# Performance work log

Hardware: AMD Instinct MI355X
Metric: run time of the kernel (lower is better)

The kernel has to match this reference:

```python
import jax, jax.numpy as jnp
import numpy as np

B, EMB, H, G, F, CH, O, OC, KT = 4096, 256, 256, 8, 96, 16, 5, 10, 5
BN_EPS = 1e-3


def _grouped_linear(x, w):
    # x: [B, I], w: [G, I//G, O//G] -> [B, O]
    b = x.shape[0]
    g, ig, og = w.shape
    xg = x.reshape(b, g, ig)
    return jnp.einsum('bgi,gio->bgo', xg, w).reshape(b, g * og)


def _gru_cell(x, h, k, rk, bias):
    # keras GRUCell, reset_after=True; gate order z, r, h; bias: [2, 3H]
    xs = x @ k + bias[0]
    hs = h @ rk + bias[1]
    xz, xr, xh = jnp.split(xs, 3, axis=-1)
    hz, hr, hh = jnp.split(hs, 3, axis=-1)
    z = jax.nn.sigmoid(xz + hz)
    r = jax.nn.sigmoid(xr + hr)
    cand = jnp.tanh(xh + r * hh)
    return z * h + (1.0 - z) * cand


def setup_inputs() -> dict:
    key = jax.random.key(0)
    ks = jax.random.split(key, 20)
    w = lambda i, shape: (jax.random.normal(ks[i], shape, dtype=jnp.float32) * 0.05)
    inp = {
        'emb': jax.random.normal(ks[0], (B, EMB), dtype=jnp.float32),
        'c0': jax.random.normal(ks[1], (B, 1, F, CH), dtype=jnp.float32),
        'df_dec_state': jax.random.normal(ks[2], (B, 2 * H), dtype=jnp.float32),
        'df_convp_buf': jax.random.normal(ks[3], (B, KT - 1, F, CH), dtype=jnp.float32),
        'w_in': w(4, (G, EMB // G, H // G)),
        'gru_k0': w(5, (H, 3 * H)),
        'gru_rk0': w(6, (H, 3 * H)),
        'gru_b0': w(7, (2, 3 * H)),
        'gru_k1': w(8, (H, 3 * H)),
        'gru_rk1': w(9, (H, 3 * H)),
        'gru_b1': w(10, (2, 3 * H)),
        'w_out': w(11, (G, H // G, (F * OC) // G)),
        'fc_a_w': w(12, (H, 1)),
        'fc_a_b': jnp.zeros((1,), dtype=jnp.float32),
        'conv_w': w(13, (KT, 1, CH // 2, OC)),  # grouped conv, groups=gcd(16,10)=2
        'pw_w': w(14, (OC, OC)),                # 1x1 pointwise, no bias
        'bn_gamma': jnp.ones((OC,), dtype=jnp.float32),
        'bn_beta': jnp.zeros((OC,), dtype=jnp.float32),
        'bn_mean': jnp.zeros((OC,), dtype=jnp.float32),
        'bn_var': jnp.ones((OC,), dtype=jnp.float32),
    }
    return inp


def reference(emb, c0, df_dec_state, df_convp_buf,
              w_in, gru_k0, gru_rk0, gru_b0, gru_k1, gru_rk1, gru_b1,
              w_out, fc_a_w, fc_a_b, conv_w, pw_w,
              bn_gamma, bn_beta, bn_mean, bn_var):
    b = emb.shape[0]
    # SqueezedGRUStep: grouped linear in-proj + ReLU
    x_in = jax.nn.relu(_grouped_linear(emb, w_in))  # [B, H]
    h0 = df_dec_state[:, :H]
    h1 = df_dec_state[:, H:]
    out0 = _gru_cell(x_in, h0, gru_k0, gru_rk0, gru_b0)
    out1 = _gru_cell(out0, h1, gru_k1, gru_rk1, gru_b1)
    new_state = jnp.concatenate([out0, out1], axis=-1)  # [B, 2H]
    c = out1 + x_in  # gru_skip = identity

    # causal conv step: concat buffer + current frame -> [B, KT, F, CH]
    x = jnp.concatenate([df_convp_buf, c0], axis=1)
    new_buf = x[:, 1:, :, :]
    # grouped conv (groups=2), kernel (KT,1), valid over the KT frames -> last frame
    xg = x.reshape(b, KT, F, 2, CH // 2)                 # [B,T,F,g,i]
    wg = conv_w.reshape(KT, CH // 2, 2, OC // 2)         # [T,i,g,o]
    y = jnp.einsum('btfgi,tigo->bfgo', xg, wg).reshape(b, F, OC)
    # separable pointwise 1x1 conv
    y = y @ pw_w
    # batch norm (inference) + relu
    inv = jax.lax.rsqrt(bn_var + BN_EPS)
    y = (y - bn_mean) * inv * bn_gamma + bn_beta
    c0_out = jax.nn.relu(y)                              # [B, F, OC]

    alpha = jax.nn.sigmoid(emb @ jnp.zeros_like(fc_a_w) + c @ fc_a_w + fc_a_b)  # [B,1]
    c_out = jnp.tanh(_grouped_linear(c, w_out)).reshape(b, F, OC)
    c_out = c_out + c0_out
    # DfOutputReshapeMF: [B,1,F,O*2] -> [B,O,1,F,2]
    coefs = c_out.reshape(b, 1, F, O, 2).transpose(0, 3, 1, 2, 4)
    return (coefs, alpha, new_state, new_buf)
```

## Files before the change

### kernel.cpp

```cpp
#include <hip/hip_runtime.h>

typedef unsigned short u16;
typedef __attribute__((ext_vector_type(8))) u16 u16x8;
typedef __attribute__((ext_vector_type(8))) __bf16 bf16x8;
typedef __attribute__((ext_vector_type(4))) float f32x4;

#define ALPHA_OFF   3932160
#define NST_OFF     3936256
#define NBUF_OFF    6033408

__device__ __forceinline__ u16 f2bf(float f) {
  unsigned u = __builtin_bit_cast(unsigned, f);
  u += 0x7fffu + ((u >> 16) & 1u);
  return (u16)(u >> 16);
}
__device__ __forceinline__ float fsig(float x) { return 1.f / (1.f + __expf(-x)); }
__device__ __forceinline__ float ftanh(float x) {
  x = fminf(15.f, fmaxf(-15.f, x));
  float e = __expf(2.f * x);
  return (e - 1.f) / (e + 1.f);
}
__device__ __forceinline__ f32x4 mfma16(u16x8 a, u16x8 b, f32x4 c) {
  return __builtin_amdgcn_mfma_f32_16x16x32_bf16(
      __builtin_bit_cast(bf16x8, a), __builtin_bit_cast(bf16x8, b), c, 0, 0, 0);
}

__global__ __launch_bounds__(256) void wprep_kernel(
    const float* __restrict__ k0, const float* __restrict__ rk0,
    const float* __restrict__ k1, const float* __restrict__ rk1,
    u16* __restrict__ kT) {
  __shared__ u16 tl[64][65];
  int nb = blockIdx.x, kb = blockIdx.y, m = blockIdx.z;
  const float* src = (m == 0) ? k0 : (m == 1) ? rk0 : (m == 2) ? k1 : rk1;
  u16* dst = kT + (size_t)m * 768 * 256;
  int tid = threadIdx.x;
  int c = tid & 63, r4 = tid >> 6;
  for (int rr = 0; rr < 64; rr += 4) {
    int k = kb * 64 + rr + r4, n = nb * 64 + c;
    tl[rr + r4][c] = f2bf(src[(size_t)k * 768 + n]);
  }
  __syncthreads();
  for (int rr = 0; rr < 64; rr += 4) {
    int n = nb * 64 + rr + r4, k = kb * 64 + c;
    dst[(size_t)n * 256 + k] = tl[c][rr + r4];
  }
}

__global__ __launch_bounds__(256) void prep_kernel(
    const float* __restrict__ emb, const float* __restrict__ dec,
    const float* __restrict__ w_in,
    float* __restrict__ x_f32, u16* __restrict__ x_q,
    u16* __restrict__ h0q, u16* __restrict__ h1q) {
  __shared__ float wl[8192];
  __shared__ float el[16][256];
  int tid = threadIdx.x, rowBase = blockIdx.x * 16;
  for (int i = tid; i < 8192; i += 256) wl[i] = w_in[i];
  for (int i = tid; i < 4096; i += 256)
    el[i >> 8][i & 255] = emb[(size_t)(rowBase + (i >> 8)) * 256 + (i & 255)];
  __syncthreads();
  int g = tid >> 5, o = tid & 31;
  for (int r = 0; r < 16; ++r) {
    float acc = 0.f;
#pragma unroll
    for (int i = 0; i < 32; ++i) acc += el[r][g * 32 + i] * wl[g * 1024 + i * 32 + o];
    acc = fmaxf(acc, 0.f);
    size_t p = (size_t)(rowBase + r) * 256 + tid;
    x_f32[p] = acc;
    x_q[p] = f2bf(acc);
  }
  for (int i = tid; i < 8192; i += 256) {
    int r = i >> 9, c = i & 511;
    float v = dec[(size_t)(rowBase + r) * 512 + c];
    if (c < 256) h0q[(size_t)(rowBase + r) * 256 + c] = f2bf(v);
    else         h1q[(size_t)(rowBase + r) * 256 + (c - 256)] = f2bf(v);
  }
}

template <int LAYER>
__global__ __launch_bounds__(256) void gru_kernel(
    const u16* __restrict__ xq, const u16* __restrict__ hq,
    const float* __restrict__ dec,
    const u16* __restrict__ kT, const u16* __restrict__ rkT,
    const float* __restrict__ bias,
    float* __restrict__ nst,
    u16* __restrict__ outq,
    const float* __restrict__ x_f32,
    float* __restrict__ c_f32) {
  __shared__ u16 lsA[2][32][40];
  __shared__ u16 lsB[2][192][40];
  int tid = threadIdx.x;
  int wave = tid >> 6, lane = tid & 63;
  int m0 = lane & 15, quad = lane >> 4;
  int rowBase = blockIdx.x * 32;
  int jz = blockIdx.y * 64;
  int cw = wave * 16;
  f32x4 az0 = {0.f, 0.f, 0.f, 0.f}, az1 = az0, ar0 = az0, ar1 = az0;
  f32x4 axh0 = az0, axh1 = az0, ahh0 = az0, ahh1 = az0;

  for (int kk = 0; kk < 8; ++kk) {
    int k0 = kk * 32;
    __syncthreads();
#pragma unroll
    for (int it = 0; it < 7; ++it) {
      int idx = tid + it * 256;
      const u16* src;
      u16* dst;
      if (idx < 256) {
        int mat = idx >> 7, r = (idx >> 2) & 31, c4 = idx & 3;
        src = (mat ? hq : xq) + (size_t)(rowBase + r) * 256 + k0 + c4 * 8;
        dst = &lsA[mat][r][c4 * 8];
      } else {
        int j = idx - 256;
        int mat = (j >= 768);
        int jm = mat ? j - 768 : j;
        int rB = jm >> 2, c4 = jm & 3;
        int n = (rB >> 6) * 256 + jz + (rB & 63);
        src = (mat ? rkT : kT) + (size_t)n * 256 + k0 + c4 * 8;
        dst = &lsB[mat][rB][c4 * 8];
      }
      *(uint4*)dst = *(const uint4*)src;
    }
    __syncthreads();
    u16x8 ax0v = *(const u16x8*)&lsA[0][m0][quad * 8];
    u16x8 ax1v = *(const u16x8*)&lsA[0][16 + m0][quad * 8];
    u16x8 ah0v = *(const u16x8*)&lsA[1][m0][quad * 8];
    u16x8 ah1v = *(const u16x8*)&lsA[1][16 + m0][quad * 8];
    u16x8 bkz = *(const u16x8*)&lsB[0][cw + m0][quad * 8];
    u16x8 bkr = *(const u16x8*)&lsB[0][64 + cw + m0][quad * 8];
    u16x8 bkh = *(const u16x8*)&lsB[0][128 + cw + m0][quad * 8];
    u16x8 brz = *(const u16x8*)&lsB[1][cw + m0][quad * 8];
    u16x8 brr = *(const u16x8*)&lsB[1][64 + cw + m0][quad * 8];
    u16x8 brh = *(const u16x8*)&lsB[1][128 + cw + m0][quad * 8];
    az0 = mfma16(ax0v, bkz, az0);  az0 = mfma16(ah0v, brz, az0);
    az1 = mfma16(ax1v, bkz, az1);  az1 = mfma16(ah1v, brz, az1);
    ar0 = mfma16(ax0v, bkr, ar0);  ar0 = mfma16(ah0v, brr, ar0);
    ar1 = mfma16(ax1v, bkr, ar1);  ar1 = mfma16(ah1v, brr, ar1);
    axh0 = mfma16(ax0v, bkh, axh0); axh1 = mfma16(ax1v, bkh, axh1);
    ahh0 = mfma16(ah0v, brh, ahh0); ahh1 = mfma16(ah1v, brh, ahh1);
  }

  int col = jz + cw + m0;
  float bz = bias[col] + bias[768 + col];
  float br = bias[256 + col] + bias[1024 + col];
  float bxh = bias[512 + col];
  float bhh = bias[1280 + col];
  const int hoff = LAYER ? 256 : 0;
#pragma unroll
  for (int t = 0; t < 2; ++t) {
    f32x4 vz = t ? az1 : az0, vr = t ? ar1 : ar0;
    f32x4 vxh = t ? axh1 : axh0, vhh = t ? ahh1 : ahh0;
#pragma unroll
    for (int i = 0; i < 4; ++i) {
      int row = rowBase + t * 16 + quad * 4 + i;
      float h = dec[(size_t)row * 512 + hoff + col];
      float z = fsig(vz[i] + bz);
      float r = fsig(vr[i] + br);
      float cand = ftanh(vxh[i] + bxh + r * (vhh[i] + bhh));
      float o = z * h + (1.f - z) * cand;
      nst[(size_t)row * 512 + hoff + col] = o;
      if (LAYER == 0) {
        outq[(size_t)row * 256 + col] = f2bf(o);
      } else {
        float c = o + x_f32[(size_t)row * 256 + col];
        c_f32[(size_t)row * 256 + col] = c;
      }
    }
  }
}

__global__ __launch_bounds__(256) void wout_kernel(
    const float* __restrict__ c_f32, const float* __restrict__ w_out,
    float* __restrict__ outc) {
  __shared__ float cs[16][256];
  int tid = threadIdx.x, rowBase = blockIdx.x * 16;
  for (int i = tid; i < 4096; i += 256)
    cs[i >> 8][i & 255] = c_f32[(size_t)(rowBase + (i >> 8)) * 256 + (i & 255)];
  __syncthreads();
  for (int flat = tid; flat < 960; flat += 256) {
    int g = flat / 120, og = flat % 120;
    float acc[16];
#pragma unroll
    for (int r = 0; r < 16; ++r) acc[r] = 0.f;
    for (int i = 0; i < 32; ++i) {
      float w = w_out[(size_t)g * 3840 + i * 120 + og];
#pragma unroll
      for (int r = 0; r < 16; ++r) acc[r] += cs[r][g * 32 + i] * w;
    }
#pragma unroll
    for (int r = 0; r < 16; ++r)
      outc[(size_t)(rowBase + r) * 960 + flat] = ftanh(acc[r]);
  }
}

__global__ __launch_bounds__(256) void head_kernel(
    const float* __restrict__ convp, const float* __restrict__ c0,
    const float* __restrict__ c_f32,
    const float* __restrict__ conv_w, const float* __restrict__ pw_w,
    const float* __restrict__ bng, const float* __restrict__ bnb,
    const float* __restrict__ bnm, const float* __restrict__ bnv,
    const float* __restrict__ fca_w, const float* __restrict__ fca_b,
    float* __restrict__ outp) {
  __shared__ float xs[5 * 96 * 16];
  __shared__ float cs[256];
  __shared__ float ybuf[96][10];
  __shared__ float cw[400];
  __shared__ float pw[100];
  __shared__ float bscale[10], bshift[10];
  __shared__ float fca[256];
  __shared__ float ared[4];
  int tid = threadIdx.x, lane = tid & 63, wave = tid >> 6;
  for (int i = tid; i < 400; i += 256) cw[i] = conv_w[i];
  if (tid < 100) pw[tid] = pw_w[tid];
  if (tid < 10) {
    float s = bng[tid] * rsqrtf(bnv[tid] + 1e-3f);
    bscale[tid] = s;
    bshift[tid] = bnb[tid] - bnm[tid] * s;
  }
  fca[tid] = fca_w[tid];
  float4* nb4 = (float4*)(outp + NBUF_OFF);
  const float4* cp4 = (const float4*)convp;
  const float4* c04 = (const float4*)c0;

  for (int rr = 0; rr < 2; ++rr) {
    int b = blockIdx.x * 2 + rr;
    __syncthreads();
    for (int i = tid; i < 1920; i += 256) {
      int t = i / 384, p = i % 384;
      float4 v = (t < 4) ? cp4[(size_t)b * 1536 + i] : c04[(size_t)b * 384 + p];
      ((float4*)xs)[i] = v;
      if (t >= 1) nb4[(size_t)b * 1536 + (size_t)(t - 1) * 384 + p] = v;
    }
    if (tid < 64) ((float4*)cs)[tid] = ((const float4*)c_f32)[(size_t)b * 64 + tid];
    __syncthreads();
    for (int u = tid; u < 960; u += 256) {
      int f = u / 10, oc = u % 10;
      int xo = (oc >= 5) ? 8 : 0;
      float acc = 0.f;
#pragma unroll
      for (int t = 0; t < 5; ++t)
#pragma unroll
        for (int i = 0; i < 8; ++i)
          acc += xs[t * 1536 + f * 16 + xo + i] * cw[t * 80 + i * 10 + oc];
      ybuf[f][oc] = acc;
    }
    float ap = cs[tid] * fca[tid];
#pragma unroll
    for (int off = 32; off > 0; off >>= 1) ap += __shfl_down(ap, off, 64);
    if (lane == 0) ared[wave] = ap;
    __syncthreads();
    if (tid == 0)
      outp[ALPHA_OFF + b] = fsig(ared[0] + ared[1] + ared[2] + ared[3] + fca_b[0]);
    float vals[4];
    int nv = 0;
    for (int u2 = tid; u2 < 480; u2 += 256) {
      int o = u2 / 96, f = u2 % 96;
#pragma unroll
      for (int q = 0; q < 2; ++q) {
        int p = o * 2 + q;
        float y2 = 0.f;
#pragma unroll
        for (int j = 0; j < 10; ++j) y2 += ybuf[f][j] * pw[j * 10 + p];
        float bnr = fmaxf(y2 * bscale[p] + bshift[p], 0.f);
        float wt = outp[(size_t)b * 960 + f * 10 + p];
        vals[nv++] = bnr + wt;
      }
    }
    __syncthreads();
    nv = 0;
    for (int u2 = tid; u2 < 480; u2 += 256) {
      int o = u2 / 96, f = u2 % 96;
      outp[(size_t)b * 960 + o * 192 + f * 2 + 0] = vals[nv++];
      outp[(size_t)b * 960 + o * 192 + f * 2 + 1] = vals[nv++];
    }
  }
}

extern "C" void kernel_launch(void* const* d_in, const int* in_sizes, int n_in,
                              void* d_out, int out_size, void* d_ws, size_t ws_size,
                              hipStream_t stream) {
  const float* emb    = (const float*)d_in[0];
  const float* c0     = (const float*)d_in[1];
  const float* dec    = (const float*)d_in[2];
  const float* convp  = (const float*)d_in[3];
  const float* w_in   = (const float*)d_in[4];
  const float* gk0    = (const float*)d_in[5];
  const float* grk0   = (const float*)d_in[6];
  const float* gb0    = (const float*)d_in[7];
  const float* gk1    = (const float*)d_in[8];
  const float* grk1   = (const float*)d_in[9];
  const float* gb1    = (const float*)d_in[10];
  const float* w_out  = (const float*)d_in[11];
  const float* fca_w  = (const float*)d_in[12];
  const float* fca_b  = (const float*)d_in[13];
  const float* conv_w = (const float*)d_in[14];
  const float* pw_w   = (const float*)d_in[15];
  const float* bng    = (const float*)d_in[16];
  const float* bnb    = (const float*)d_in[17];
  const float* bnm    = (const float*)d_in[18];
  const float* bnv    = (const float*)d_in[19];
  float* out = (float*)d_out;
  char* ws = (char*)d_ws;
  float* x_f32 = (float*)(ws + 0);
  float* c_f32 = (float*)(ws + 4194304);
  u16*   x_q   = (u16*)(ws + 8388608);
  u16*   h0q   = (u16*)(ws + 10485760);
  u16*   h1q   = (u16*)(ws + 12582912);
  u16*   o0q   = (u16*)(ws + 14680064);
  u16*   kT    = (u16*)(ws + 16777216);

  wprep_kernel<<<dim3(12, 4, 4), 256, 0, stream>>>(gk0, grk0, gk1, grk1, kT);
  prep_kernel<<<dim3(256), 256, 0, stream>>>(emb, dec, w_in, x_f32, x_q, h0q, h1q);
  gru_kernel<0><<<dim3(128, 4), 256, 0, stream>>>(x_q, h0q, dec, kT, kT + 196608,
                                                  gb0, out + NST_OFF, o0q, nullptr, nullptr);
  gru_kernel<1><<<dim3(128, 4), 256, 0, stream>>>(o0q, h1q, dec, kT + 2 * 196608, kT + 3 * 196608,
                                                  gb1, out + NST_OFF, nullptr, x_f32, c_f32);
  wout_kernel<<<dim3(256), 256, 0, stream>>>(c_f32, w_out, out);
  head_kernel<<<dim3(2048), 256, 0, stream>>>(convp, c0, c_f32, conv_w, pw_w,
                                              bng, bnb, bnm, bnv, fca_w, fca_b, out);
}
```

Before: 346.4 us.

## Concatenate GRU K-dim, double-buffer via global_load_lds, bf16 conv staging

The input and recurrent weights are concatenated along K into one [768,512] bf16 matrix per layer. Activations are packed as [x|h] rows, so the GRU GEMM becomes a single K=512 loop with 64-row tiles, double-buffered through direct global-to-LDS loads. The fp32 x copy is dropped and the skip connection reads the bf16 x instead, which adds rounding error. The head kernel moves to one batch row per block, stages the conv input as bf16 in LDS and restructures the conv so each thread computes five outputs.

Result: slower. 357.3 us (+3.1%).

```diff
diff --git a/kernel.cpp b/kernel.cpp
--- a/kernel.cpp
+++ b/kernel.cpp
@@ -13,6 +13,9 @@
   unsigned u = __builtin_bit_cast(unsigned, f);
   u += 0x7fffu + ((u >> 16) & 1u);
   return (u16)(u >> 16);
+}
+__device__ __forceinline__ float bf2f(u16 v) {
+  return __builtin_bit_cast(float, (unsigned)v << 16);
 }
 __device__ __forceinline__ float fsig(float x) { return 1.f / (1.f + __expf(-x)); }
 __device__ __forceinline__ float ftanh(float x) {
@@ -24,33 +27,36 @@
   return __builtin_amdgcn_mfma_f32_16x16x32_bf16(
       __builtin_bit_cast(bf16x8, a), __builtin_bit_cast(bf16x8, b), c, 0, 0, 0);
 }
+__device__ __forceinline__ void gload16(const void* g, void* l) {
+  __builtin_amdgcn_global_load_lds(
+      (const __attribute__((address_space(1))) void*)g,
+      (__attribute__((address_space(3))) void*)l, 16, 0, 0);
+}
 
 __global__ __launch_bounds__(256) void wprep_kernel(
-    const float* __restrict__ k0, const float* __restrict__ rk0,
-    const float* __restrict__ k1, const float* __restrict__ rk1,
-    u16* __restrict__ kT) {
+    const float* __restrict__ gk0, const float* __restrict__ grk0,
+    const float* __restrict__ gk1, const float* __restrict__ grk1,
+    u16* __restrict__ W2) {
   __shared__ u16 tl[64][65];
-  int nb = blockIdx.x, kb = blockIdx.y, m = blockIdx.z;
-  const float* src = (m == 0) ? k0 : (m == 1) ? rk0 : (m == 2) ? k1 : rk1;
-  u16* dst = kT + (size_t)m * 768 * 256;
-  int tid = threadIdx.x;
-  int c = tid & 63, r4 = tid >> 6;
+  int nb = blockIdx.x, kb = blockIdx.y, L = blockIdx.z;
+  const float* src = (kb < 4) ? (L ? gk1 : gk0) : (L ? grk1 : grk0);
+  int kbase = (kb & 3) * 64;
+  u16* dst = W2 + (size_t)L * 768 * 512;
+  int tid = threadIdx.x, c = tid & 63, r4 = tid >> 6;
   for (int rr = 0; rr < 64; rr += 4) {
-    int k = kb * 64 + rr + r4, n = nb * 64 + c;
+    int k = kbase + rr + r4, n = nb * 64 + c;
     tl[rr + r4][c] = f2bf(src[(size_t)k * 768 + n]);
   }
   __syncthreads();
   for (int rr = 0; rr < 64; rr += 4) {
     int n = nb * 64 + rr + r4, k = kb * 64 + c;
-    dst[(size_t)n * 256 + k] = tl[c][rr + r4];
+    dst[(size_t)n * 512 + k] = tl[c][rr + r4];
   }
 }
 
 __global__ __launch_bounds__(256) void prep_kernel(
     const float* __restrict__ emb, const float* __restrict__ dec,
-    const float* __restrict__ w_in,
-    float* __restrict__ x_f32, u16* __restrict__ x_q,
-    u16* __restrict__ h0q, u16* __restrict__ h1q) {
+    const float* __restrict__ w_in, u16* __restrict__ A0, u16* __restrict__ A1) {
   __shared__ float wl[8192];
   __shared__ float el[16][256];
   int tid = threadIdx.x, rowBase = blockIdx.x * 16;
@@ -63,80 +69,70 @@
     float acc = 0.f;
 #pragma unroll
     for (int i = 0; i < 32; ++i) acc += el[r][g * 32 + i] * wl[g * 1024 + i * 32 + o];
-    acc = fmaxf(acc, 0.f);
-    size_t p = (size_t)(rowBase + r) * 256 + tid;
-    x_f32[p] = acc;
-    x_q[p] = f2bf(acc);
+    A0[(size_t)(rowBase + r) * 512 + tid] = f2bf(fmaxf(acc, 0.f));
   }
   for (int i = tid; i < 8192; i += 256) {
     int r = i >> 9, c = i & 511;
-    float v = dec[(size_t)(rowBase + r) * 512 + c];
-    if (c < 256) h0q[(size_t)(rowBase + r) * 256 + c] = f2bf(v);
-    else         h1q[(size_t)(rowBase + r) * 256 + (c - 256)] = f2bf(v);
+    u16 q = f2bf(dec[(size_t)(rowBase + r) * 512 + c]);
+    if (c < 256) A0[(size_t)(rowBase + r) * 512 + 256 + c] = q;
+    else         A1[(size_t)(rowBase + r) * 512 + c] = q;
   }
 }
 
 template <int LAYER>
 __global__ __launch_bounds__(256) void gru_kernel(
-    const u16* __restrict__ xq, const u16* __restrict__ hq,
+    const u16* __restrict__ Ain,
+    const u16* __restrict__ W2,
     const float* __restrict__ dec,
-    const u16* __restrict__ kT, const u16* __restrict__ rkT,
     const float* __restrict__ bias,
     float* __restrict__ nst,
-    u16* __restrict__ outq,
-    const float* __restrict__ x_f32,
+    u16* __restrict__ a1out,
+    const u16* __restrict__ xbf,
     float* __restrict__ c_f32) {
-  __shared__ u16 lsA[2][32][40];
-  __shared__ u16 lsB[2][192][40];
-  int tid = threadIdx.x;
-  int wave = tid >> 6, lane = tid & 63;
+  __shared__ __align__(16) u16 lsA[2][64][32];
+  __shared__ __align__(16) u16 lsB[2][3][64][32];
+  int tid = threadIdx.x, lane = tid & 63, wave = tid >> 6;
   int m0 = lane & 15, quad = lane >> 4;
-  int rowBase = blockIdx.x * 32;
-  int jz = blockIdx.y * 64;
-  int cw = wave * 16;
-  f32x4 az0 = {0.f, 0.f, 0.f, 0.f}, az1 = az0, ar0 = az0, ar1 = az0;
-  f32x4 axh0 = az0, axh1 = az0, ahh0 = az0, ahh1 = az0;
-
-  for (int kk = 0; kk < 8; ++kk) {
-    int k0 = kk * 32;
+  int rowBase = blockIdx.x * 64, jz = blockIdx.y * 64, cw = wave * 16;
+  f32x4 acc[4][4];
+#pragma unroll
+  for (int gi = 0; gi < 4; ++gi)
+#pragma unroll
+    for (int rb = 0; rb < 4; ++rb) acc[gi][rb] = (f32x4){0.f, 0.f, 0.f, 0.f};
+
+  int rS = tid >> 2, qS = tid & 3;
+  auto stage = [&](int buf, int k0) {
+    gload16(Ain + (size_t)(rowBase + rS) * 512 + k0 + qS * 8, &lsA[buf][rS][qS * 8]);
+#pragma unroll
+    for (int g = 0; g < 3; ++g)
+      gload16(W2 + (size_t)(g * 256 + jz + rS) * 512 + k0 + qS * 8,
+              &lsB[buf][g][rS][qS * 8]);
+  };
+
+  stage(0, 0);
+  for (int step = 0; step < 16; ++step) {
     __syncthreads();
-#pragma unroll
-    for (int it = 0; it < 7; ++it) {
-      int idx = tid + it * 256;
-      const u16* src;
-      u16* dst;
-      if (idx < 256) {
-        int mat = idx >> 7, r = (idx >> 2) & 31, c4 = idx & 3;
-        src = (mat ? hq : xq) + (size_t)(rowBase + r) * 256 + k0 + c4 * 8;
-        dst = &lsA[mat][r][c4 * 8];
-      } else {
-        int j = idx - 256;
-        int mat = (j >= 768);
-        int jm = mat ? j - 768 : j;
-        int rB = jm >> 2, c4 = jm & 3;
-        int n = (rB >> 6) * 256 + jz + (rB & 63);
-        src = (mat ? rkT : kT) + (size_t)n * 256 + k0 + c4 * 8;
-        dst = &lsB[mat][rB][c4 * 8];
-      }
-      *(uint4*)dst = *(const uint4*)src;
-    }
-    __syncthreads();
-    u16x8 ax0v = *(const u16x8*)&lsA[0][m0][quad * 8];
-    u16x8 ax1v = *(const u16x8*)&lsA[0][16 + m0][quad * 8];
-    u16x8 ah0v = *(const u16x8*)&lsA[1][m0][quad * 8];
-    u16x8 ah1v = *(const u16x8*)&lsA[1][16 + m0][quad * 8];
-    u16x8 bkz = *(const u16x8*)&lsB[0][cw + m0][quad * 8];
-    u16x8 bkr = *(const u16x8*)&lsB[0][64 + cw + m0][quad * 8];
-    u16x8 bkh = *(const u16x8*)&lsB[0][128 + cw + m0][quad * 8];
-    u16x8 brz = *(const u16x8*)&lsB[1][cw + m0][quad * 8];
-    u16x8 brr = *(const u16x8*)&lsB[1][64 + cw + m0][quad * 8];
-    u16x8 brh = *(const u16x8*)&lsB[1][128 + cw + m0][quad * 8];
-    az0 = mfma16(ax0v, bkz, az0);  az0 = mfma16(ah0v, brz, az0);
-    az1 = mfma16(ax1v, bkz, az1);  az1 = mfma16(ah1v, brz, az1);
-    ar0 = mfma16(ax0v, bkr, ar0);  ar0 = mfma16(ah0v, brr, ar0);
-    ar1 = mfma16(ax1v, bkr, ar1);  ar1 = mfma16(ah1v, brr, ar1);
-    axh0 = mfma16(ax0v, bkh, axh0); axh1 = mfma16(ax1v, bkh, axh1);
-    ahh0 = mfma16(ah0v, brh, ahh0); ahh1 = mfma16(ah1v, brh, ahh1);
+    if (step < 15) stage((step & 1) ^ 1, (step + 1) * 32);
+    int cur = step & 1;
+    u16x8 av[4], bv[3];
+#pragma unroll
+    for (int rb = 0; rb < 4; ++rb)
+      av[rb] = *(const u16x8*)&lsA[cur][rb * 16 + m0][quad * 8];
+#pragma unroll
+    for (int g = 0; g < 3; ++g)
+      bv[g] = *(const u16x8*)&lsB[cur][g][cw + m0][quad * 8];
+#pragma unroll
+    for (int rb = 0; rb < 4; ++rb) {
+      acc[0][rb] = mfma16(av[rb], bv[0], acc[0][rb]);
+      acc[1][rb] = mfma16(av[rb], bv[1], acc[1][rb]);
+    }
+    if (step < 8) {
+#pragma unroll
+      for (int rb = 0; rb < 4; ++rb) acc[2][rb] = mfma16(av[rb], bv[2], acc[2][rb]);
+    } else {
+#pragma unroll
+      for (int rb = 0; rb < 4; ++rb) acc[3][rb] = mfma16(av[rb], bv[2], acc[3][rb]);
+    }
   }
 
   int col = jz + cw + m0;
@@ -146,22 +142,20 @@
   float bhh = bias[1280 + col];
   const int hoff = LAYER ? 256 : 0;
 #pragma unroll
-  for (int t = 0; t < 2; ++t) {
-    f32x4 vz = t ? az1 : az0, vr = t ? ar1 : ar0;
-    f32x4 vxh = t ? axh1 : axh0, vhh = t ? ahh1 : ahh0;
+  for (int rb = 0; rb < 4; ++rb) {
 #pragma unroll
     for (int i = 0; i < 4; ++i) {
-      int row = rowBase + t * 16 + quad * 4 + i;
+      int row = rowBase + rb * 16 + quad * 4 + i;
       float h = dec[(size_t)row * 512 + hoff + col];
-      float z = fsig(vz[i] + bz);
-      float r = fsig(vr[i] + br);
-      float cand = ftanh(vxh[i] + bxh + r * (vhh[i] + bhh));
+      float z = fsig(acc[0][rb][i] + bz);
+      float r = fsig(acc[1][rb][i] + br);
+      float cand = ftanh(acc[2][rb][i] + bxh + r * (acc[3][rb][i] + bhh));
       float o = z * h + (1.f - z) * cand;
       nst[(size_t)row * 512 + hoff + col] = o;
       if (LAYER == 0) {
-        outq[(size_t)row * 256 + col] = f2bf(o);
+        a1out[(size_t)row * 512 + col] = f2bf(o);
       } else {
-        float c = o + x_f32[(size_t)row * 256 + col];
+        float c = o + bf2f(xbf[(size_t)row * 512 + col]);
         c_f32[(size_t)row * 256 + col] = c;
       }
     }
@@ -200,15 +194,14 @@
     const float* __restrict__ bnm, const float* __restrict__ bnv,
     const float* __restrict__ fca_w, const float* __restrict__ fca_b,
     float* __restrict__ outp) {
-  __shared__ float xs[5 * 96 * 16];
-  __shared__ float cs[256];
+  __shared__ __align__(16) u16 xs[5 * 96 * 16];
   __shared__ float ybuf[96][10];
   __shared__ float cw[400];
   __shared__ float pw[100];
   __shared__ float bscale[10], bshift[10];
-  __shared__ float fca[256];
   __shared__ float ared[4];
   int tid = threadIdx.x, lane = tid & 63, wave = tid >> 6;
+  int b = blockIdx.x;
   for (int i = tid; i < 400; i += 256) cw[i] = conv_w[i];
   if (tid < 100) pw[tid] = pw_w[tid];
   if (tid < 10) {
@@ -216,62 +209,65 @@
     bscale[tid] = s;
     bshift[tid] = bnb[tid] - bnm[tid] * s;
   }
-  fca[tid] = fca_w[tid];
   float4* nb4 = (float4*)(outp + NBUF_OFF);
   const float4* cp4 = (const float4*)convp;
   const float4* c04 = (const float4*)c0;
 
-  for (int rr = 0; rr < 2; ++rr) {
-    int b = blockIdx.x * 2 + rr;
-    __syncthreads();
-    for (int i = tid; i < 1920; i += 256) {
-      int t = i / 384, p = i % 384;
-      float4 v = (t < 4) ? cp4[(size_t)b * 1536 + i] : c04[(size_t)b * 384 + p];
-      ((float4*)xs)[i] = v;
-      if (t >= 1) nb4[(size_t)b * 1536 + (size_t)(t - 1) * 384 + p] = v;
-    }
-    if (tid < 64) ((float4*)cs)[tid] = ((const float4*)c_f32)[(size_t)b * 64 + tid];
-    __syncthreads();
-    for (int u = tid; u < 960; u += 256) {
-      int f = u / 10, oc = u % 10;
-      int xo = (oc >= 5) ? 8 : 0;
-      float acc = 0.f;
-#pragma unroll
-      for (int t = 0; t < 5; ++t)
-#pragma unroll
-        for (int i = 0; i < 8; ++i)
-          acc += xs[t * 1536 + f * 16 + xo + i] * cw[t * 80 + i * 10 + oc];
-      ybuf[f][oc] = acc;
-    }
-    float ap = cs[tid] * fca[tid];
-#pragma unroll
-    for (int off = 32; off > 0; off >>= 1) ap += __shfl_down(ap, off, 64);
-    if (lane == 0) ared[wave] = ap;
-    __syncthreads();
-    if (tid == 0)
-      outp[ALPHA_OFF + b] = fsig(ared[0] + ared[1] + ared[2] + ared[3] + fca_b[0]);
-    float vals[4];
-    int nv = 0;
-    for (int u2 = tid; u2 < 480; u2 += 256) {
-      int o = u2 / 96, f = u2 % 96;
-#pragma unroll
-      for (int q = 0; q < 2; ++q) {
-        int p = o * 2 + q;
-        float y2 = 0.f;
-#pragma unroll
-        for (int j = 0; j < 10; ++j) y2 += ybuf[f][j] * pw[j * 10 + p];
-        float bnr = fmaxf(y2 * bscale[p] + bshift[p], 0.f);
-        float wt = outp[(size_t)b * 960 + f * 10 + p];
-        vals[nv++] = bnr + wt;
+  for (int i = tid; i < 1920; i += 256) {
+    int t = i / 384, p = i % 384;
+    float4 v = (t < 4) ? cp4[(size_t)b * 1536 + i] : c04[(size_t)b * 384 + p];
+    if (t >= 1) nb4[(size_t)b * 1536 + (size_t)(t - 1) * 384 + p] = v;
+    ushort4 q;
+    q.x = f2bf(v.x); q.y = f2bf(v.y); q.z = f2bf(v.z); q.w = f2bf(v.w);
+    ((ushort4*)xs)[i] = q;
+  }
+  float ap = c_f32[(size_t)b * 256 + tid] * fca_w[tid];
+#pragma unroll
+  for (int off = 32; off > 0; off >>= 1) ap += __shfl_down(ap, off, 64);
+  if (lane == 0) ared[wave] = ap;
+  __syncthreads();
+  if (tid == 0)
+    outp[ALPHA_OFF + b] = fsig(ared[0] + ared[1] + ared[2] + ared[3] + fca_b[0]);
+  if (tid < 192) {
+    int f = tid >> 1, half = tid & 1;
+    float a5[5] = {0.f, 0.f, 0.f, 0.f, 0.f};
+#pragma unroll
+    for (int t = 0; t < 5; ++t) {
+      u16x8 xv = *(const u16x8*)&xs[t * 1536 + f * 16 + half * 8];
+#pragma unroll
+      for (int i = 0; i < 8; ++i) {
+        float xf = bf2f(xv[i]);
+#pragma unroll
+        for (int j = 0; j < 5; ++j)
+          a5[j] += xf * cw[t * 80 + i * 10 + half * 5 + j];
       }
     }
-    __syncthreads();
-    nv = 0;
-    for (int u2 = tid; u2 < 480; u2 += 256) {
-      int o = u2 / 96, f = u2 % 96;
-      outp[(size_t)b * 960 + o * 192 + f * 2 + 0] = vals[nv++];
-      outp[(size_t)b * 960 + o * 192 + f * 2 + 1] = vals[nv++];
-    }
+#pragma unroll
+    for (int j = 0; j < 5; ++j) ybuf[f][half * 5 + j] = a5[j];
+  }
+  __syncthreads();
+  float vals[4];
+  int nv = 0;
+  for (int u2 = tid; u2 < 480; u2 += 256) {
+    int o = u2 / 96, f = u2 % 96;
+#pragma unroll
+    for (int q = 0; q < 2; ++q) {
+      int p = o * 2 + q;
+      float y2 = 0.f;
+#pragma unroll
+      for (int j = 0; j < 10; ++j) y2 += ybuf[f][j] * pw[j * 10 + p];
+      float bnr = fmaxf(y2 * bscale[p] + bshift[p], 0.f);
+      float wt = outp[(size_t)b * 960 + f * 10 + p];
+      vals[nv++] = bnr + wt;
+    }
+  }
+  __syncthreads();
+  nv = 0;
+  for (int u2 = tid; u2 < 480; u2 += 256) {
+    int o = u2 / 96, f = u2 % 96;
+    *(float2*)&outp[(size_t)b * 960 + o * 192 + f * 2] =
+        make_float2(vals[nv], vals[nv + 1]);
+    nv += 2;
   }
 }
 
@@ -300,21 +296,18 @@
   const float* bnv    = (const float*)d_in[19];
   float* out = (float*)d_out;
   char* ws = (char*)d_ws;
-  float* x_f32 = (float*)(ws + 0);
-  float* c_f32 = (float*)(ws + 4194304);
-  u16*   x_q   = (u16*)(ws + 8388608);
-  u16*   h0q   = (u16*)(ws + 10485760);
-  u16*   h1q   = (u16*)(ws + 12582912);
-  u16*   o0q   = (u16*)(ws + 14680064);
-  u16*   kT    = (u16*)(ws + 16777216);
-
-  wprep_kernel<<<dim3(12, 4, 4), 256, 0, stream>>>(gk0, grk0, gk1, grk1, kT);
-  prep_kernel<<<dim3(256), 256, 0, stream>>>(emb, dec, w_in, x_f32, x_q, h0q, h1q);
-  gru_kernel<0><<<dim3(128, 4), 256, 0, stream>>>(x_q, h0q, dec, kT, kT + 196608,
-                                                  gb0, out + NST_OFF, o0q, nullptr, nullptr);
-  gru_kernel<1><<<dim3(128, 4), 256, 0, stream>>>(o0q, h1q, dec, kT + 2 * 196608, kT + 3 * 196608,
-                                                  gb1, out + NST_OFF, nullptr, x_f32, c_f32);
+  u16*   A0    = (u16*)(ws + 0);
+  u16*   A1    = (u16*)(ws + 4194304);
+  float* c_f32 = (float*)(ws + 8388608);
+  u16*   W2    = (u16*)(ws + 12582912);
+
+  wprep_kernel<<<dim3(12, 8, 2), 256, 0, stream>>>(gk0, grk0, gk1, grk1, W2);
+  prep_kernel<<<dim3(256), 256, 0, stream>>>(emb, dec, w_in, A0, A1);
+  gru_kernel<0><<<dim3(64, 4), 256, 0, stream>>>(A0, W2, dec, gb0,
+                                                 out + NST_OFF, A1, nullptr, nullptr);
+  gru_kernel<1><<<dim3(64, 4), 256, 0, stream>>>(A1, W2 + 768 * 512, dec, gb1,
+                                                 out + NST_OFF, nullptr, A0, c_f32);
   wout_kernel<<<dim3(256), 256, 0, stream>>>(c_f32, w_out, out);
-  head_kernel<<<dim3(2048), 256, 0, stream>>>(convp, c0, c_f32, conv_w, pw_w,
+  head_kernel<<<dim3(4096), 256, 0, stream>>>(convp, c0, c_f32, conv_w, pw_w,
                                               bng, bnb, bnm, bnv, fca_w, fca_b, out);
 }
```
